# Optimization experiments

Hardware: AMD Instinct MI355X
Metric: run time of the kernel (lower is better)

The kernel has to match this reference:

```python
import jax, jax.numpy as jnp
import numpy as np

INPUT_DIM = 362
HIDDEN = 256
STYLE_NUM = 60
OUTFIT_NUM = 49710
BATCH = 16384


def setup_inputs() -> dict:
    key = jax.random.key(0)
    ks = jax.random.split(key, 12)
    f32 = jnp.float32
    return {
        "i_feature": jax.random.normal(ks[0], (BATCH, INPUT_DIM), f32),
        "j_feature": jax.random.normal(ks[1], (BATCH, INPUT_DIM), f32),
        "k_feature": jax.random.normal(ks[2], (BATCH, INPUT_DIM), f32),
        # top_emb / bottom_emb Linear params (stored transposed: x @ W + b)
        "W_top": jax.random.normal(ks[3], (INPUT_DIM, HIDDEN), f32) * 0.05,
        "b_top": jnp.zeros((HIDDEN,), f32),
        "W_bot": jax.random.normal(ks[4], (INPUT_DIM, HIDDEN), f32) * 0.05,
        "b_bot": jnp.zeros((HIDDEN,), f32),
        # NMF factors (forward relu_'s them in place; we relu on use)
        "P_nmf": jax.random.normal(ks[5], (2 * INPUT_DIM, STYLE_NUM), f32),
        "N_nmf": jax.random.normal(ks[6], (2 * INPUT_DIM, STYLE_NUM), f32),
        "H1_nmf": jax.random.normal(ks[7], (STYLE_NUM, OUTFIT_NUM), f32),
        "H2_nmf": jax.random.normal(ks[8], (STYLE_NUM, OUTFIT_NUM), f32),
        "matirx_pos": jax.random.uniform(ks[9], (2 * INPUT_DIM, OUTFIT_NUM), f32),
        "matirx_neg": jax.random.uniform(ks[10], (2 * INPUT_DIM, OUTFIT_NUM), f32),
    }


def _emb(x, W, b):
    # nn.Sequential(Linear, Sigmoid)
    return jax.nn.sigmoid(x @ W + b)


def _style_score(i_f, j_f, styles, W_top, b_top, W_bot, b_bot):
    # Vectorized version of the per-sample loop:
    # squared-distance argmin codebook lookup + gather + rowwise dot.
    outfit = jnp.concatenate([i_f, j_f], axis=1)  # [B, 2D]
    # mean over feature dim of (x - s)^2; constant 1/(2D) scale does not change argmin
    d2 = (jnp.sum(outfit * outfit, axis=1, keepdims=True)
          - 2.0 * (outfit @ styles)
          + jnp.sum(styles * styles, axis=0, keepdims=True))  # [B, S]
    idx = jnp.argmin(d2, axis=1)                               # [B]
    sel = styles.T[idx]                                        # [B, 2D] gather
    top, bot = sel[:, :INPUT_DIM], sel[:, INPUT_DIM:]
    # diag(matmul) == rowwise dot
    return jnp.sum(_emb(top, W_top, b_top) * _emb(bot, W_bot, b_bot), axis=1)  # [B]


def reference(i_feature, j_feature, k_feature, W_top, b_top, W_bot, b_bot,
              P_nmf, N_nmf, H1_nmf, H2_nmf, matirx_pos, matirx_neg):
    Ti = _emb(i_feature, W_top, b_top)   # [B, H]
    Bj = _emb(j_feature, W_bot, b_bot)   # [B, H]
    Bk = _emb(k_feature, W_bot, b_bot)   # [B, H]
    # torch.diag(matmul(Ti, Bj.T)) == rowwise dot (avoids [B,B] intermediate)
    ij_score = jnp.sum(Ti * Bj, axis=1)  # [B]
    ik_score = jnp.sum(Ti * Bk, axis=1)  # [B]

    # forward does relu_ on .data before use
    P = jnp.maximum(P_nmf, 0.0)
    N = jnp.maximum(N_nmf, 0.0)
    H1 = jnp.maximum(H1_nmf, 0.0)
    H2 = jnp.maximum(H2_nmf, 0.0)

    style_ij = _style_score(i_feature, j_feature, P, W_top, b_top, W_bot, b_bot)
    style_ik = _style_score(i_feature, k_feature, N, W_top, b_top, W_bot, b_bot)

    # -mean(log(sigmoid(d))) computed stably
    loss1 = -jnp.mean(jax.nn.log_sigmoid(ij_score - ik_score))
    loss2 = -jnp.mean(jax.nn.log_sigmoid(style_ij - style_ik))
    loss3 = jnp.mean(jnp.square(matirx_pos - P @ H1)
                     + jnp.square(matirx_neg - N @ H2))
    loss = loss1 + loss2 + 0.1 * loss3

    ij_ik = jnp.stack([ij_score, ik_score], axis=1)  # [B, 2]
    auc = jnp.mean((jnp.argmax(ij_ik, axis=1) == 0).astype(jnp.float32))
    return (loss, loss1, loss2, loss3, auc)
```

## Files before the change

### kernel.cpp

```cpp
#include <hip/hip_runtime.h>
#include <math.h>

#define BATCH 16384
#define IND   362
#define KP    384
#define HID   256
#define STY   60
#define NOUT  49710
#define OUTP  49792
#define D2    724
#define D2P   768
#define L3_BLOCKS 17871

typedef __bf16 bf16x8 __attribute__((ext_vector_type(8)));
typedef float  floatx4 __attribute__((ext_vector_type(4)));

__device__ inline floatx4 mfma16(bf16x8 a, bf16x8 b, floatx4 c) {
  return __builtin_amdgcn_mfma_f32_16x16x32_bf16(a, b, c, 0, 0, 0);
}

__device__ inline unsigned short f32_to_bf16(float x) {
  unsigned int u = __float_as_uint(x);
  unsigned int r = (u + 0x7FFFu + ((u >> 16) & 1u)) >> 16;
  return (unsigned short)r;
}

__device__ inline float sigm_fast(float x) { return 1.0f / (1.0f + __expf(-x)); }
__device__ inline float softplusf(float z) { return fmaxf(z, 0.0f) + log1pf(expf(-fabsf(z))); }


__global__ void k_conv_feat(const float* __restrict__ fi, const float* __restrict__ fj,
                            const float* __restrict__ fk, unsigned short* __restrict__ fbf) {
  int row = blockIdx.x;
  int f = blockIdx.y;
  const float* src = (f == 0) ? fi : (f == 1 ? fj : fk);
  unsigned short* dst = fbf + ((size_t)f * BATCH + row) * KP;
  for (int d = threadIdx.x; d < KP; d += blockDim.x) {
    float v = (d < IND) ? src[(size_t)row * IND + d] : 0.0f;
    dst[d] = f32_to_bf16(v);
  }
}

__global__ void k_conv_w(const float* __restrict__ Wt, const float* __restrict__ Wb,
                         unsigned short* __restrict__ wbfT) {
  int h = blockIdx.x;
  int m = blockIdx.y;
  const float* W = m ? Wb : Wt;
  unsigned short* dst = wbfT + ((size_t)m * HID + h) * KP;
  for (int k = threadIdx.x; k < KP; k += blockDim.x) {
    float v = (k < IND) ? W[(size_t)k * HID + h] : 0.0f;
    dst[k] = f32_to_bf16(v);
  }
}

__global__ void k_conv_pn(const float* __restrict__ P, const float* __restrict__ N,
                          unsigned short* __restrict__ pnbf, unsigned short* __restrict__ pnbfT) {
  int d = blockIdx.x;
  int m = blockIdx.y;
  int s = threadIdx.x;
  const float* M = m ? N : P;
  float v = (d < D2 && s < STY) ? fmaxf(M[(size_t)d * STY + s], 0.0f) : 0.0f;
  unsigned short b = f32_to_bf16(v);
  pnbf[((size_t)m * D2P + d) * 64 + s] = b;
  int k = (d < IND) ? d : (d < D2 ? d + 22 : (d < 746 ? d - IND : d));
  pnbfT[((size_t)m * 64 + s) * D2P + k] = b;
}

__global__ void k_conv_h(const float* __restrict__ H1, const float* __restrict__ H2,
                         unsigned short* __restrict__ hbfT) {
  int o = blockIdx.x * 256 + threadIdx.x;
  int m = blockIdx.y;
  if (o >= OUTP) return;
  const float* H = m ? H2 : H1;
  unsigned short* dst = hbfT + ((size_t)m * OUTP + o) * 64;
  bool ov = (o < NOUT);
  #pragma unroll
  for (int g = 0; g < 8; g++) {
    unsigned int wv[4];
    #pragma unroll
    for (int e = 0; e < 4; e++) {
      int kk = g * 8 + e * 2;
      float lo = (ov && kk < STY)     ? fmaxf(H[(size_t)kk * NOUT + o], 0.0f) : 0.0f;
      float hi = (ov && kk + 1 < STY) ? fmaxf(H[(size_t)(kk + 1) * NOUT + o], 0.0f) : 0.0f;
      wv[e] = (unsigned)f32_to_bf16(lo) | ((unsigned)f32_to_bf16(hi) << 16);
    }
    uint4 v; v.x = wv[0]; v.y = wv[1]; v.z = wv[2]; v.w = wv[3];
    *(uint4*)(dst + g * 8) = v;
  }
}

__global__ __launch_bounds__(256) void k_style_scalar(
    const float* __restrict__ Pn, const float* __restrict__ Nn,
    const float* __restrict__ Wt, const float* __restrict__ btop,
    const float* __restrict__ Wb, const float* __restrict__ bbot,
    float* __restrict__ ss, float* __restrict__ cn) {
  int s  = blockIdx.x % STY;
  int mt = blockIdx.x / STY;
  const float* M = mt ? Nn : Pn;
  __shared__ float sel[D2];
  __shared__ float shr[4];
  int t = threadIdx.x;
  float cnp = 0.0f;
  for (int d = t; d < D2; d += 256) {
    float v = fmaxf(M[(size_t)d * STY + s], 0.0f);
    sel[d] = v;
    cnp += v * v;
  }
  __syncthreads();
  float at = btop[t], ab = bbot[t];
  for (int d = 0; d < IND; d++) at = fmaf(sel[d],        Wt[(size_t)d * HID + t], at);
  for (int d = 0; d < IND; d++) ab = fmaf(sel[IND + d],  Wb[(size_t)d * HID + t], ab);
  float prod = (1.0f / (1.0f + expf(-at))) * (1.0f / (1.0f + expf(-ab)));
  for (int off = 32; off > 0; off >>= 1) prod += __shfl_xor(prod, off);
  if ((t & 63) == 0) shr[t >> 6] = prod;
  __syncthreads();
  if (t == 0) ss[mt * 64 + s] = shr[0] + shr[1] + shr[2] + shr[3];
  __syncthreads();
  for (int off = 32; off > 0; off >>= 1) cnp += __shfl_xor(cnp, off);
  if ((t & 63) == 0) shr[t >> 6] = cnp;
  __syncthreads();
  if (t == 0) cn[mt * 64 + s] = shr[0] + shr[1] + shr[2] + shr[3];
}

__global__ __launch_bounds__(256) void k_emb(
    const unsigned short* __restrict__ fbf, const unsigned short* __restrict__ wbfT,
    const float* __restrict__ btop, const float* __restrict__ bbot,
    float* __restrict__ sIJ, float* __restrict__ sIK) {
  int w = threadIdx.x >> 6, lane = threadIdx.x & 63;
  int m = lane & 15, q = lane >> 4;
  int r0 = blockIdx.x * 64 + w * 16;
  int hb = blockIdx.y * 128;
  const unsigned short* fi = fbf + (size_t)(r0 + m) * KP + q * 8;
  const unsigned short* fj = fi + (size_t)BATCH * KP;
  const unsigned short* fk = fj + (size_t)BATCH * KP;
  floatx4 accI[8], accJ[8], accK[8];
  #pragma unroll
  for (int nt = 0; nt < 8; nt++) {
    accI[nt] = (floatx4){0.f, 0.f, 0.f, 0.f};
    accJ[nt] = (floatx4){0.f, 0.f, 0.f, 0.f};
    accK[nt] = (floatx4){0.f, 0.f, 0.f, 0.f};
  }
  for (int kc = 0; kc < 12; kc++) {
    bf16x8 ai = *(const bf16x8*)(fi + kc * 32);
    bf16x8 aj = *(const bf16x8*)(fj + kc * 32);
    bf16x8 ak = *(const bf16x8*)(fk + kc * 32);
    #pragma unroll
    for (int nt = 0; nt < 8; nt++) {
      int n = hb + nt * 16 + m;
      const unsigned short* wp = wbfT + (size_t)n * KP + kc * 32 + q * 8;
      bf16x8 bt8 = *(const bf16x8*)(wp);
      bf16x8 bb8 = *(const bf16x8*)(wp + (size_t)HID * KP);
      accI[nt] = mfma16(ai, bt8, accI[nt]);
      accJ[nt] = mfma16(aj, bb8, accJ[nt]);
      accK[nt] = mfma16(ak, bb8, accK[nt]);
    }
  }
  float sij[4] = {0.f, 0.f, 0.f, 0.f}, sik[4] = {0.f, 0.f, 0.f, 0.f};
  #pragma unroll
  for (int nt = 0; nt < 8; nt++) {
    int n = hb + nt * 16 + m;
    float vbt = btop[n], vbb = bbot[n];
    #pragma unroll
    for (int reg = 0; reg < 4; reg++) {
      float ti = sigm_fast(accI[nt][reg] + vbt);
      float tj = sigm_fast(accJ[nt][reg] + vbb);
      float tk = sigm_fast(accK[nt][reg] + vbb);
      sij[reg] += ti * tj;
      sik[reg] += ti * tk;
    }
  }
  #pragma unroll
  for (int reg = 0; reg < 4; reg++) {
    for (int off = 1; off < 16; off <<= 1) {
      sij[reg] += __shfl_xor(sij[reg], off);
      sik[reg] += __shfl_xor(sik[reg], off);
    }
  }
  if (m == 0) {
    #pragma unroll
    for (int reg = 0; reg < 4; reg++) {
      int row = r0 + q * 4 + reg;
      atomicAdd(&sIJ[row], sij[reg]);
      atomicAdd(&sIK[row], sik[reg]);
    }
  }
}

__global__ __launch_bounds__(256) void k_style_assign(
    const unsigned short* __restrict__ fbf, const unsigned short* __restrict__ pnbfT,
    const float* __restrict__ cn, const float* __restrict__ ss,
    float* __restrict__ stIJ, float* __restrict__ stIK) {
  int w = threadIdx.x >> 6, lane = threadIdx.x & 63;
  int m = lane & 15, q = lane >> 4;
  int mat = w & 1;
  int r0 = blockIdx.x * 32 + (w >> 1) * 16;
  const unsigned short* fA = fbf + (size_t)(r0 + m) * KP + q * 8;
  const unsigned short* fB = fA + (size_t)(1 + mat) * BATCH * KP;
  const unsigned short* Bp = pnbfT + (size_t)mat * 64 * D2P + q * 8;
  floatx4 acc[4];
  #pragma unroll
  for (int nt = 0; nt < 4; nt++) acc[nt] = (floatx4){0.f, 0.f, 0.f, 0.f};
  for (int kc = 0; kc < 24; kc++) {
    bf16x8 a = (kc < 12) ? *(const bf16x8*)(fA + kc * 32)
                         : *(const bf16x8*)(fB + (kc - 12) * 32);
    #pragma unroll
    for (int nt = 0; nt < 4; nt++) {
      bf16x8 b = *(const bf16x8*)(Bp + (size_t)(nt * 16 + m) * D2P + kc * 32);
      acc[nt] = mfma16(a, b, acc[nt]);
    }
  }
  const float* cnm = cn + mat * 64;
  float bv[4]; int bi[4];
  #pragma unroll
  for (int reg = 0; reg < 4; reg++) { bv[reg] = __builtin_inff(); bi[reg] = 1 << 30; }
  #pragma unroll
  for (int nt = 0; nt < 4; nt++) {
    int s = nt * 16 + m;
    float c = cnm[s & 63];
    #pragma unroll
    for (int reg = 0; reg < 4; reg++) {
      float d2 = (s < STY) ? (c - 2.0f * acc[nt][reg]) : __builtin_inff();
      if (d2 < bv[reg] || (d2 == bv[reg] && s < bi[reg])) { bv[reg] = d2; bi[reg] = s; }
    }
  }
  for (int off = 1; off < 16; off <<= 1) {
    #pragma unroll
    for (int reg = 0; reg < 4; reg++) {
      float ov = __shfl_xor(bv[reg], off);
      int   oi = __shfl_xor(bi[reg], off);
      if (ov < bv[reg] || (ov == bv[reg] && oi < bi[reg])) { bv[reg] = ov; bi[reg] = oi; }
    }
  }
  if (m == 0) {
    float* dst = mat ? stIK : stIJ;
    const float* ssm = ss + mat * 64;
    #pragma unroll
    for (int reg = 0; reg < 4; reg++) dst[r0 + q * 4 + reg] = ssm[bi[reg]];
  }
}

__global__ __launch_bounds__(256) void k_loss3(
    const unsigned short* __restrict__ pnbf, const unsigned short* __restrict__ hbfT,
    const float* __restrict__ mp, const float* __restrict__ mn,
    float* __restrict__ partial) {
  const int NT_D = 46;
  const long NT_O = 777;
  const long TT = NT_D * NT_O;
  int w = threadIdx.x >> 6, lane = threadIdx.x & 63;
  int m = lane & 15, q = lane >> 4;
  long wid = (long)blockIdx.x * 4 + w;
  float local = 0.0f;
  {
    int mat = (wid >= TT) ? 1 : 0;
    long rem = wid - (long)mat * TT;
    int dt = (int)(rem % NT_D);
    int ot = (int)(rem / NT_D);
    int d0 = dt * 16, o0 = ot * 64;
    const unsigned short* A = pnbf + (size_t)mat * D2P * 64 + (size_t)(d0 + m) * 64 + q * 8;
    const unsigned short* B = hbfT + (size_t)mat * OUTP * 64 + q * 8;
    const float* M = mat ? mn : mp;
    floatx4 acc[4];
    #pragma unroll
    for (int nt = 0; nt < 4; nt++) acc[nt] = (floatx4){0.f, 0.f, 0.f, 0.f};
    #pragma unroll
    for (int kc = 0; kc < 2; kc++) {
      bf16x8 a = *(const bf16x8*)(A + kc * 32);
      #pragma unroll
      for (int nt = 0; nt < 4; nt++) {
        bf16x8 b = *(const bf16x8*)(B + (size_t)(o0 + nt * 16 + m) * 64 + kc * 32);
        acc[nt] = mfma16(a, b, acc[nt]);
      }
    }
    #pragma unroll
    for (int nt = 0; nt < 4; nt++) {
      int o = o0 + nt * 16 + m;
      #pragma unroll
      for (int reg = 0; reg < 4; reg++) {
        int d = d0 + q * 4 + reg;
        if (d < D2 && o < NOUT) {
          float e = M[(size_t)d * NOUT + o] - acc[nt][reg];
          local += e * e;
        }
      }
    }
  }
  for (int off = 32; off > 0; off >>= 1) local += __shfl_xor(local, off);
  __shared__ float shp[4];
  if (lane == 0) shp[w] = local;
  __syncthreads();
  if (threadIdx.x == 0) partial[blockIdx.x] = shp[0] + shp[1] + shp[2] + shp[3];
}

__global__ __launch_bounds__(256) void k_final(
    const float* __restrict__ sIJ, const float* __restrict__ sIK,
    const float* __restrict__ stIJ, const float* __restrict__ stIK,
    const float* __restrict__ l3partial, float* __restrict__ out) {
  int t = threadIdx.x;
  float l1 = 0.f, l2 = 0.f, ac = 0.f;
  for (int r = t; r < BATCH; r += 256) {
    float dij = sIJ[r] - sIK[r];
    l1 += softplusf(-dij);
    if (dij >= 0.0f) ac += 1.0f;
    float dst = stIJ[r] - stIK[r];
    l2 += softplusf(-dst);
  }
  double l3 = 0.0;
  for (int p = t; p < L3_BLOCKS; p += 256) l3 += (double)l3partial[p];
  __shared__ float sh1[4], sh2[4], sh3[4];
  __shared__ double sh4[4];
  for (int off = 32; off > 0; off >>= 1) {
    l1 += __shfl_xor(l1, off);
    l2 += __shfl_xor(l2, off);
    ac += __shfl_xor(ac, off);
    l3 += __shfl_xor(l3, off);
  }
  if ((t & 63) == 0) { sh1[t >> 6] = l1; sh2[t >> 6] = l2; sh3[t >> 6] = ac; sh4[t >> 6] = l3; }
  __syncthreads();
  if (t == 0) {
    double L1 = 0, L2 = 0, AC = 0, L3 = 0;
    for (int i = 0; i < 4; i++) { L1 += sh1[i]; L2 += sh2[i]; AC += sh3[i]; L3 += sh4[i]; }
    L1 /= BATCH; L2 /= BATCH; AC /= BATCH;
    L3 /= ((double)D2 * (double)NOUT);
    out[0] = (float)(L1 + L2 + 0.1 * L3);
    out[1] = (float)L1;
    out[2] = (float)L2;
    out[3] = (float)L3;
    out[4] = (float)AC;
  }
}

extern "C" void kernel_launch(void* const* d_in, const int* in_sizes, int n_in,
                              void* d_out, int out_size, void* d_ws, size_t ws_size,
                              hipStream_t stream) {
  (void)in_sizes; (void)n_in; (void)out_size; (void)ws_size;
  const float* i_f  = (const float*)d_in[0];
  const float* j_f  = (const float*)d_in[1];
  const float* k_f  = (const float*)d_in[2];
  const float* W_t  = (const float*)d_in[3];
  const float* b_t  = (const float*)d_in[4];
  const float* W_b  = (const float*)d_in[5];
  const float* b_b  = (const float*)d_in[6];
  const float* P_n  = (const float*)d_in[7];
  const float* N_n  = (const float*)d_in[8];
  const float* H1   = (const float*)d_in[9];
  const float* H2   = (const float*)d_in[10];
  const float* Mp   = (const float*)d_in[11];
  const float* Mn   = (const float*)d_in[12];
  float* out = (float*)d_out;
  char* ws = (char*)d_ws;

  const size_t OFF_FBF   = 0;
  const size_t OFF_WBFT  = OFF_FBF  + (size_t)3 * BATCH * KP * 2;
  const size_t OFF_PNBF  = OFF_WBFT + (size_t)2 * HID * KP * 2;
  const size_t OFF_PNBFT = OFF_PNBF + (size_t)2 * D2P * 64 * 2;
  const size_t OFF_HBFT  = OFF_PNBFT+ (size_t)2 * 64 * D2P * 2;
  const size_t OFF_SIJ   = OFF_HBFT + (size_t)2 * OUTP * 64 * 2;
  const size_t OFF_SIK   = OFF_SIJ  + (size_t)BATCH * 4;
  const size_t OFF_STIJ  = OFF_SIK  + (size_t)BATCH * 4;
  const size_t OFF_STIK  = OFF_STIJ + (size_t)BATCH * 4;
  const size_t OFF_SS    = OFF_STIK + (size_t)BATCH * 4;
  const size_t OFF_CN    = OFF_SS   + 512;
  const size_t OFF_L3P   = OFF_CN   + 512;

  unsigned short* fbf   = (unsigned short*)(ws + OFF_FBF);
  unsigned short* wbfT  = (unsigned short*)(ws + OFF_WBFT);
  unsigned short* pnbf  = (unsigned short*)(ws + OFF_PNBF);
  unsigned short* pnbfT = (unsigned short*)(ws + OFF_PNBFT);
  unsigned short* hbfT  = (unsigned short*)(ws + OFF_HBFT);
  float*  sIJ  = (float*)(ws + OFF_SIJ);
  float*  sIK  = (float*)(ws + OFF_SIK);
  float*  stIJ = (float*)(ws + OFF_STIJ);
  float*  stIK = (float*)(ws + OFF_STIK);
  float*  ss   = (float*)(ws + OFF_SS);
  float*  cn   = (float*)(ws + OFF_CN);
  float*  l3p  = (float*)(ws + OFF_L3P);

  hipMemsetAsync(ws + OFF_SIJ, 0, (size_t)BATCH * 4 * 2, stream);

  k_conv_feat<<<dim3(BATCH, 3), 128, 0, stream>>>(i_f, j_f, k_f, fbf);
  k_conv_w   <<<dim3(HID, 2),  128, 0, stream>>>(W_t, W_b, wbfT);
  k_conv_pn  <<<dim3(D2P, 2),   64, 0, stream>>>(P_n, N_n, pnbf, pnbfT);
  k_conv_h   <<<dim3(195, 2),  256, 0, stream>>>(H1, H2, hbfT);

  k_style_scalar<<<120, 256, 0, stream>>>(P_n, N_n, W_t, b_t, W_b, b_b, ss, cn);
  k_emb         <<<dim3(BATCH / 64, 2), 256, 0, stream>>>(fbf, wbfT, b_t, b_b, sIJ, sIK);
  k_style_assign<<<BATCH / 32, 256, 0, stream>>>(fbf, pnbfT, cn, ss, stIJ, stIK);
  k_loss3       <<<L3_BLOCKS, 256, 0, stream>>>(pnbf, hbfT, Mp, Mn, l3p);
  k_final       <<<1, 256, 0, stream>>>(sIJ, sIK, stIJ, stIK, l3p, out);
}
```

Baseline: 772.9 us.

## Restructure loss3 into per-strip blocks reusing H tiles and swap MFMA operands

The loss3 kernel now assigns one block per 64-column output strip and matrix. It loads the H fragments once into registers and loops over d-tiles, so H is no longer reloaded for every 16x64 tile. MFMA operands are swapped so each lane's accumulator lies along contiguous output columns, which allows vectorized loads of the reference matrix. Separately, the feature conversion kernel is rewritten so each thread converts 8 elements and issues one 16-byte store. The risk is fewer, longer blocks (1554 of them) and uneven per-wave work, which could reduce memory-level parallelism on a bandwidth-bound pass over the ~290 MB matrices.

After: 674.4 us. 1.15x faster.

```diff
diff --git a/kernel.cpp b/kernel.cpp
--- a/kernel.cpp
+++ b/kernel.cpp
@@ -10,10 +10,12 @@
 #define OUTP  49792
 #define D2    724
 #define D2P   768
-#define L3_BLOCKS 17871
+#define NSTRIP 777
+#define L3_BLOCKS (2 * NSTRIP)
 
 typedef __bf16 bf16x8 __attribute__((ext_vector_type(8)));
 typedef float  floatx4 __attribute__((ext_vector_type(4)));
+typedef float  floatx2 __attribute__((ext_vector_type(2)));
 
 __device__ inline floatx4 mfma16(bf16x8 a, bf16x8 b, floatx4 c) {
   return __builtin_amdgcn_mfma_f32_16x16x32_bf16(a, b, c, 0, 0, 0);
@@ -29,16 +31,29 @@
 __device__ inline float softplusf(float z) { return fmaxf(z, 0.0f) + log1pf(expf(-fabsf(z))); }
 
 
-__global__ void k_conv_feat(const float* __restrict__ fi, const float* __restrict__ fj,
-                            const float* __restrict__ fk, unsigned short* __restrict__ fbf) {
-  int row = blockIdx.x;
-  int f = blockIdx.y;
+__global__ __launch_bounds__(256) void k_conv_feat(
+    const float* __restrict__ fi, const float* __restrict__ fj,
+    const float* __restrict__ fk, unsigned short* __restrict__ fbf) {
+  long u = (long)blockIdx.x * 256 + threadIdx.x;
+  const long TOT = (long)3 * BATCH * 48;
+  if (u >= TOT) return;
+  int g = (int)(u % 48);
+  long rf = u / 48;
+  int row = (int)(rf % BATCH);
+  int f = (int)(rf / BATCH);
   const float* src = (f == 0) ? fi : (f == 1 ? fj : fk);
-  unsigned short* dst = fbf + ((size_t)f * BATCH + row) * KP;
-  for (int d = threadIdx.x; d < KP; d += blockDim.x) {
-    float v = (d < IND) ? src[(size_t)row * IND + d] : 0.0f;
-    dst[d] = f32_to_bf16(v);
-  }
+  int d0 = g * 8;
+  const float* sp = src + (size_t)row * IND + d0;
+  unsigned int wv[4];
+  #pragma unroll
+  for (int e = 0; e < 4; e++) {
+    int dd = d0 + 2 * e;
+    float lo = (dd < IND)     ? sp[2 * e]     : 0.0f;
+    float hi = (dd + 1 < IND) ? sp[2 * e + 1] : 0.0f;
+    wv[e] = (unsigned)f32_to_bf16(lo) | ((unsigned)f32_to_bf16(hi) << 16);
+  }
+  uint4 v; v.x = wv[0]; v.y = wv[1]; v.z = wv[2]; v.w = wv[3];
+  *(uint4*)(fbf + ((size_t)f * BATCH + row) * KP + d0) = v;
 }
 
 __global__ void k_conv_w(const float* __restrict__ Wt, const float* __restrict__ Wb,
@@ -243,43 +258,65 @@
     const unsigned short* __restrict__ pnbf, const unsigned short* __restrict__ hbfT,
     const float* __restrict__ mp, const float* __restrict__ mn,
     float* __restrict__ partial) {
-  const int NT_D = 46;
-  const long NT_O = 777;
-  const long TT = NT_D * NT_O;
   int w = threadIdx.x >> 6, lane = threadIdx.x & 63;
   int m = lane & 15, q = lane >> 4;
-  long wid = (long)blockIdx.x * 4 + w;
+  int strip = blockIdx.x % NSTRIP;
+  int mat   = blockIdx.x / NSTRIP;
+  int o0 = strip * 64;
+  const float* M = mat ? mn : mp;
+  const unsigned short* Hb = hbfT + (size_t)mat * OUTP * 64;
+  const unsigned short* Pb = pnbf + (size_t)mat * D2P * 64;
+
+  bf16x8 a[4][2];
+  #pragma unroll
+  for (int t = 0; t < 4; t++)
+    #pragma unroll
+    for (int kc = 0; kc < 2; kc++)
+      a[t][kc] = *(const bf16x8*)(Hb + (size_t)(o0 + t * 16 + m) * 64 + kc * 32 + q * 8);
+
+  int dt0 = w * 12;
+  int ntile = (w < 3) ? 12 : 10;
+  bool full = (o0 + 64 <= NOUT);
   float local = 0.0f;
-  {
-    int mat = (wid >= TT) ? 1 : 0;
-    long rem = wid - (long)mat * TT;
-    int dt = (int)(rem % NT_D);
-    int ot = (int)(rem / NT_D);
-    int d0 = dt * 16, o0 = ot * 64;
-    const unsigned short* A = pnbf + (size_t)mat * D2P * 64 + (size_t)(d0 + m) * 64 + q * 8;
-    const unsigned short* B = hbfT + (size_t)mat * OUTP * 64 + q * 8;
-    const float* M = mat ? mn : mp;
+
+  for (int it = 0; it < ntile; it++) {
+    int d0 = (dt0 + it) * 16;
+    const unsigned short* bp = Pb + (size_t)(d0 + m) * 64 + q * 8;
+    bf16x8 b0 = *(const bf16x8*)(bp);
+    bf16x8 b1 = *(const bf16x8*)(bp + 32);
     floatx4 acc[4];
     #pragma unroll
-    for (int nt = 0; nt < 4; nt++) acc[nt] = (floatx4){0.f, 0.f, 0.f, 0.f};
-    #pragma unroll
-    for (int kc = 0; kc < 2; kc++) {
-      bf16x8 a = *(const bf16x8*)(A + kc * 32);
-      #pragma unroll
-      for (int nt = 0; nt < 4; nt++) {
-        bf16x8 b = *(const bf16x8*)(B + (size_t)(o0 + nt * 16 + m) * 64 + kc * 32);
-        acc[nt] = mfma16(a, b, acc[nt]);
-      }
-    }
-    #pragma unroll
-    for (int nt = 0; nt < 4; nt++) {
-      int o = o0 + nt * 16 + m;
-      #pragma unroll
-      for (int reg = 0; reg < 4; reg++) {
-        int d = d0 + q * 4 + reg;
-        if (d < D2 && o < NOUT) {
-          float e = M[(size_t)d * NOUT + o] - acc[nt][reg];
-          local += e * e;
+    for (int t = 0; t < 4; t++) {
+      acc[t] = (floatx4){0.f, 0.f, 0.f, 0.f};
+      acc[t] = mfma16(a[t][0], b0, acc[t]);
+      acc[t] = mfma16(a[t][1], b1, acc[t]);
+    }
+    int d = d0 + m;
+    if (d < D2) {
+      const float* Mrow = M + (size_t)d * NOUT;
+      if (full) {
+        #pragma unroll
+        for (int t = 0; t < 4; t++) {
+          int ob = o0 + t * 16 + q * 4;
+          floatx2 m01 = *(const floatx2*)(Mrow + ob);
+          floatx2 m23 = *(const floatx2*)(Mrow + ob + 2);
+          float e0 = m01[0] - acc[t][0];
+          float e1 = m01[1] - acc[t][1];
+          float e2 = m23[0] - acc[t][2];
+          float e3 = m23[1] - acc[t][3];
+          local += e0 * e0 + e1 * e1 + e2 * e2 + e3 * e3;
+        }
+      } else {
+        #pragma unroll
+        for (int t = 0; t < 4; t++) {
+          int ob = o0 + t * 16 + q * 4;
+          #pragma unroll
+          for (int reg = 0; reg < 4; reg++) {
+            if (ob + reg < NOUT) {
+              float e = Mrow[ob + reg] - acc[t][reg];
+              local += e * e;
+            }
+          }
         }
       }
     }
@@ -377,7 +414,7 @@
 
   hipMemsetAsync(ws + OFF_SIJ, 0, (size_t)BATCH * 4 * 2, stream);
 
-  k_conv_feat<<<dim3(BATCH, 3), 128, 0, stream>>>(i_f, j_f, k_f, fbf);
+  k_conv_feat<<<(3 * BATCH * 48 + 255) / 256, 256, 0, stream>>>(i_f, j_f, k_f, fbf);
   k_conv_w   <<<dim3(HID, 2),  128, 0, stream>>>(W_t, W_b, wbfT);
   k_conv_pn  <<<dim3(D2P, 2),   64, 0, stream>>>(P_n, N_n, pnbf, pnbfT);
   k_conv_h   <<<dim3(195, 2),  256, 0, stream>>>(H1, H2, hbfT);
```
